# Kernel optimization log

Hardware: AMD Instinct MI355X
Metric: run time of the kernel (lower is better)

Reference implementation:

```python
import jax, jax.numpy as jnp
import numpy as np

D_MODEL = 2048
N_HEADS = 16
HEAD_DIM = D_MODEL // N_HEADS  # 128
B, S, PAST = 2, 2048, 2048


def setup_inputs() -> dict:
    key = jax.random.key(0)
    ks = jax.random.split(key, 7)
    sc = 0.02
    return {
        "x": jax.random.normal(ks[0], (B, S, D_MODEL), dtype=jnp.float32),
        "past_k": jax.random.normal(ks[1], (B, N_HEADS, PAST, HEAD_DIM), dtype=jnp.float32),
        "past_v": jax.random.normal(ks[2], (B, N_HEADS, PAST, HEAD_DIM), dtype=jnp.float32),
        "Wq": jax.random.normal(ks[3], (D_MODEL, D_MODEL), dtype=jnp.float32) * sc,
        "Wk": jax.random.normal(ks[4], (D_MODEL, D_MODEL), dtype=jnp.float32) * sc,
        "Wv": jax.random.normal(ks[5], (D_MODEL, D_MODEL), dtype=jnp.float32) * sc,
        "Wo": jax.random.normal(ks[6], (D_MODEL, D_MODEL), dtype=jnp.float32) * sc,
    }


def reference(x, past_k, past_v, Wq, Wk, Wv, Wo):
    b, s, d = x.shape
    # nn.Linear(bias=False): y = x @ W.T ; split heads -> (B, H, S, hd)
    def proj_heads(W):
        return (x @ W.T).reshape(b, s, N_HEADS, HEAD_DIM).transpose(0, 2, 1, 3)
    q = proj_heads(Wq)
    k = proj_heads(Wk)
    v = proj_heads(Wv)
    # KV-cache append along sequence axis
    k = jnp.concatenate([past_k, k], axis=2)  # (B, H, full_S, hd)
    v = jnp.concatenate([past_v, v], axis=2)
    present = (k, v)
    full_s = k.shape[2]
    scores = jnp.einsum("bhqd,bhkd->bhqk", q, k) / (HEAD_DIM ** 0.5)
    # causal mask: query i (global pos past+i) may attend keys j <= past+i
    offset = full_s - s
    qi = jnp.arange(s)[:, None]
    kj = jnp.arange(full_s)[None, :]
    mask = kj > (qi + offset)  # triu with diagonal = full_s - s + 1
    scores = jnp.where(mask[None, None], -jnp.inf, scores)
    attn = jax.nn.softmax(scores, axis=-1)
    out = jnp.einsum("bhqk,bhkd->bhqd", attn, v)
    out = out.transpose(0, 2, 1, 3).reshape(b, s, d)
    output = out @ Wo.T
    return output, present
```

## Files before the change

kernel.cpp:

```cpp
#include <hip/hip_runtime.h>
#include <hip/hip_bf16.h>
#include <stdint.h>

typedef __attribute__((ext_vector_type(8))) short bf16x8;
typedef __attribute__((ext_vector_type(4))) float f32x4;
typedef __attribute__((ext_vector_type(16))) float f32x16;
typedef unsigned short u16;
typedef unsigned int u32;
typedef const __attribute__((address_space(1))) u32* gp_t;
typedef __attribute__((address_space(3))) u32* lp_t;

#define HD 128
#define NH 16
#define SEQ 2048
#define PASTN 2048
#define FULLS 4096
#define DM 2048

__device__ __forceinline__ u16 f2b(float f){
  union { float f; u32 u; } v; v.f = f;
  return (u16)((v.u + 0x7fffu + ((v.u >> 16) & 1u)) >> 16);
}
__device__ __forceinline__ float b2f(u16 b){
  union { u32 u; float f; } v; v.u = ((u32)b) << 16;
  return v.f;
}
__device__ __forceinline__ u32 cvtpk(float lo, float hi){
  u32 r; asm("v_cvt_pk_bf16_f32 %0, %1, %2" : "=v"(r) : "v"(lo), "v"(hi)); return r;
}
__device__ __forceinline__ f32x16 zero16(){ f32x16 z = {}; return z; }

__global__ void k_conv5(const float* __restrict__ sx,
                        const float* __restrict__ s1, const float* __restrict__ s2,
                        const float* __restrict__ s3, const float* __restrict__ s4,
                        u16* __restrict__ dx,
                        u16* __restrict__ d1, u16* __restrict__ d2,
                        u16* __restrict__ d3, u16* __restrict__ d4)
{
  const int total = 2097152 + 4 * 1048576;
  int i = blockIdx.x * blockDim.x + threadIdx.x;
  int stride = gridDim.x * blockDim.x;
  for (; i < total; i += stride){
    const float* s; u16* d; int off;
    if (i < 2097152){ s = sx; d = dx; off = i; }
    else {
      int t = i - 2097152;
      int seg = t >> 20; off = t & 1048575;
      s = (seg == 0) ? s1 : (seg == 1) ? s2 : (seg == 2) ? s3 : s4;
      d = (seg == 0) ? d1 : (seg == 1) ? d2 : (seg == 2) ? d3 : d4;
    }
    float4 v = ((const float4*)s)[off];
    ushort4 o = { f2b(v.x), f2b(v.y), f2b(v.z), f2b(v.w) };
    ((ushort4*)d)[off] = o;
  }
}

__global__ __launch_bounds__(512, 1)
void k_qkv_fused(const u16* __restrict__ A,
                 const u16* __restrict__ Bq, const u16* __restrict__ Bk,
                 const u16* __restrict__ Bv,
                 u16* __restrict__ qb, u16* __restrict__ kbb,
                 u16* __restrict__ vtb,
                 float* __restrict__ outk, float* __restrict__ outv,
                 const float* __restrict__ pk, const float* __restrict__ pv)
{
  __shared__ char LDS[131072];
  const int bx = blockIdx.x;
  const int tid = threadIdx.x;

  if (bx >= 384){
    if (bx < 448){
      for (int i = (bx - 384) * 512 + tid; i < 2097152; i += 32768){
        int g = i * 4;
        int c = g & 127;
        int r = g >> 7;
        int bh = r >> 11;
        int s = r & 2047;
        long dst = ((long)bh * FULLS + s) * HD + c;
        float4 v = ((const float4*)pk)[i];
        *(float4*)(outk + dst) = v;
        ushort4 o = { f2b(v.x), f2b(v.y), f2b(v.z), f2b(v.w) };
        *(ushort4*)(kbb + dst) = o;
      }
    } else {
      float* ldsF = (float*)LDS;
      for (int cc = 0; cc < 16; cc++){
        int c = ((bx - 448) << 4) + cc;
        int bh = c >> 5, s0 = (c & 31) << 6;
        const float* src = pv + ((long)bh * PASTN + s0) * HD;
        float* dsv = outv + ((long)bh * FULLS + s0) * HD;
#pragma unroll
        for (int p = 0; p < 4; p++){
          int idx = tid + p * 512;
          int row = idx >> 5, c4 = (idx & 31) << 2;
          float4 v = *(const float4*)(src + row * HD + c4);
          *(float4*)(dsv + row * HD + c4) = v;
          ldsF[row * 129 + c4 + 0] = v.x;
          ldsF[row * 129 + c4 + 1] = v.y;
          ldsF[row * 129 + c4 + 2] = v.z;
          ldsF[row * 129 + c4 + 3] = v.w;
        }
        __syncthreads();
        int d = tid >> 2, sb = (tid & 3) << 4;
        u16* dst = vtb + ((long)bh * HD + d) * FULLS + s0 + sb;
#pragma unroll
        for (int g = 0; g < 4; g++){
          ushort4 o = { f2b(ldsF[(sb + g * 4 + 0) * 129 + d]),
                        f2b(ldsF[(sb + g * 4 + 1) * 129 + d]),
                        f2b(ldsF[(sb + g * 4 + 2) * 129 + d]),
                        f2b(ldsF[(sb + g * 4 + 3) * 129 + d]) };
          *(ushort4*)(dst + g * 4) = o;
        }
        __syncthreads();
      }
    }
    return;
  }

  const int w = tid >> 6, l = tid & 63;
  const int wm = w >> 2, wn = w & 3;
  const int which = bx >> 7;
  const int r0 = bx & 127;
  const int m0 = (r0 & 15) * 256;
  const int n0s = (r0 >> 4) * 256;
  const u16* Bm = (which == 0) ? Bq : (which == 1) ? Bk : Bv;

  const int aoff0 = (((l >> 4) * 16) ^ ((l & 7) << 4));
  const int aoff1 = ((64 + (l >> 4) * 16) ^ ((l & 7) << 4));
  const char* ArdB = LDS + wm * 16384 + (l & 15) * 128;
  const char* BrdB = LDS + 65536 + (wn >> 1) * 16384 + (wn & 1) * 8192 + (l & 15) * 128;

  const int Pa = tid * 16, Pb = tid * 16 + 8192;
  const int ra = Pa >> 7, rb = Pb >> 7;
  const int sro1 = ra * 2048 + ((((Pa & 127) ^ ((ra & 7) << 4))) >> 1);
  const int sro2 = rb * 2048 + ((((Pb & 127) ^ ((rb & 7) << 4))) >> 1);
  char* sd1 = LDS + w * 1024;
  char* sd2 = LDS + w * 1024 + 8192;

  f32x4 acc[8][4] = {};

#define GLDS(SRC, DST) __builtin_amdgcn_global_load_lds((gp_t)(const void*)(SRC), (lp_t)(void*)(DST), 16, 0, 0)
#define STG(MAT, ROWB, C, REG) { const u16* s_ = (MAT) + (long)(ROWB) * 2048 + (C) * 64; \
    GLDS(s_ + sro1, sd1 + (REG)); GLDS(s_ + sro2, sd2 + (REG)); }
#define RDB(DST, PAR) { _Pragma("unroll") for (int nf = 0; nf < 4; nf++){ \
      DST[nf*2]   = *(const bf16x8*)(BrdB + (PAR)*32768 + nf*2048 + aoff0); \
      DST[nf*2+1] = *(const bf16x8*)(BrdB + (PAR)*32768 + nf*2048 + aoff1); } }
#define RDA(PAR, MF) \
      a0 = *(const bf16x8*)(ArdB + (PAR)*32768 + (MF)*2048 + aoff0); \
      a1 = *(const bf16x8*)(ArdB + (PAR)*32768 + (MF)*2048 + aoff1); \
      a2 = *(const bf16x8*)(ArdB + (PAR)*32768 + (MF+1)*2048 + aoff0); \
      a3 = *(const bf16x8*)(ArdB + (PAR)*32768 + (MF+1)*2048 + aoff1);
#define BARW { __builtin_amdgcn_s_barrier(); \
      asm volatile("s_waitcnt lgkmcnt(0)" ::: "memory"); \
      __builtin_amdgcn_sched_barrier(0); }
#define MM(BF, MF) { __builtin_amdgcn_s_setprio(1); \
      _Pragma("unroll") for (int nf = 0; nf < 4; nf++){ \
        acc[MF][nf]   = __builtin_amdgcn_mfma_f32_16x16x32_bf16(a0, BF[nf*2],   acc[MF][nf],   0,0,0); \
        acc[MF][nf]   = __builtin_amdgcn_mfma_f32_16x16x32_bf16(a1, BF[nf*2+1], acc[MF][nf],   0,0,0); \
        acc[MF+1][nf] = __builtin_amdgcn_mfma_f32_16x16x32_bf16(a2, BF[nf*2],   acc[MF+1][nf], 0,0,0); \
        acc[MF+1][nf] = __builtin_amdgcn_mfma_f32_16x16x32_bf16(a3, BF[nf*2+1], acc[MF+1][nf], 0,0,0); } \
      __builtin_amdgcn_s_setprio(0); }

  STG(A,  m0,        0, 0);
  STG(A,  m0 + 128,  0, 16384);
  STG(Bm, n0s,       0, 65536);
  STG(Bm, n0s + 128, 0, 81920);
  STG(Bm, n0s,       1, 98304);
  STG(Bm, n0s + 128, 1, 114688);
  asm volatile("s_waitcnt vmcnt(4)" ::: "memory");
  __builtin_amdgcn_s_barrier();

  for (int i = 0; i < 16; ++i){
    const int c1 = 2 * i + 1;
    const int cn = 2 * i + 2;
    const bool nlast = (i < 15);
    bf16x8 b0[8], b1[8];
    bf16x8 a0, a1, a2, a3;

    RDB(b0, 0); RDA(0, 0);
    STG(A, m0, c1, 32768);
    BARW; MM(b0, 0);
    __builtin_amdgcn_s_barrier();

    RDA(0, 2);
    STG(A, m0 + 128, c1, 49152);
    BARW; MM(b0, 2);
    __builtin_amdgcn_s_barrier();

    RDA(0, 4);
    if (nlast) STG(Bm, n0s, cn, 65536);
    BARW; MM(b0, 4);
    __builtin_amdgcn_s_barrier();

    RDA(0, 6);
    if (nlast) STG(Bm, n0s + 128, cn, 81920);
    BARW; MM(b0, 6);
    if (nlast) { asm volatile("s_waitcnt vmcnt(4)" ::: "memory"); }
    else       { asm volatile("s_waitcnt vmcnt(0)" ::: "memory"); }
    __builtin_amdgcn_s_barrier();

    RDB(b1, 1); RDA(1, 0);
    if (nlast) STG(A, m0, cn, 0);
    BARW; MM(b1, 0);
    __builtin_amdgcn_s_barrier();

    RDA(1, 2);
    if (nlast) STG(A, m0 + 128, cn, 16384);
    BARW; MM(b1, 2);
    __builtin_amdgcn_s_barrier();

    RDA(1, 4);
    if (nlast) STG(Bm, n0s, cn + 1, 98304);
    BARW; MM(b1, 4);
    __builtin_amdgcn_s_barrier();

    RDA(1, 6);
    if (nlast) STG(Bm, n0s + 128, cn + 1, 114688);
    BARW; MM(b1, 6);
    if (nlast) { asm volatile("s_waitcnt vmcnt(4)" ::: "memory"); }
    __builtin_amdgcn_s_barrier();
  }

#undef MM
#undef BARW
#undef RDA
#undef RDB
#undef STG
#undef GLDS

  const int rbase = m0 + wm * 128 + ((l >> 4) << 2);
  const int cb2 = n0s + wn * 64 + (l & 15);
#pragma unroll
  for (int mf = 0; mf < 8; mf++){
#pragma unroll
    for (int nf = 0; nf < 4; nf++){
      const int nl = cb2 + nf * 16;
      const int h = nl >> 7, dd = nl & 127;
      if (which == 2){
        const int mm = rbase + mf * 16;
        const int b = mm >> 11, s = mm & 2047;
        const int bh = b * NH + h;
        ushort4 pkv = { f2b(acc[mf][nf][0]), f2b(acc[mf][nf][1]), f2b(acc[mf][nf][2]), f2b(acc[mf][nf][3]) };
        *(ushort4*)(vtb + ((long)bh * HD + dd) * FULLS + PASTN + s) = pkv;
#pragma unroll
        for (int r = 0; r < 4; r++){
          long idx = ((long)bh * FULLS + PASTN + s + r) * HD + dd;
          outv[idx] = acc[mf][nf][r];
        }
      } else if (which == 1){
#pragma unroll
        for (int r = 0; r < 4; r++){
          const int mm = rbase + mf * 16 + r;
          const int b = mm >> 11, s = mm & 2047;
          long idx = (((long)(b * NH + h)) * FULLS + PASTN + s) * HD + dd;
          float v = acc[mf][nf][r];
          kbb[idx] = f2b(v);
          outk[idx] = v;
        }
      } else {
#pragma unroll
        for (int r = 0; r < 4; r++){
          const int mm = rbase + mf * 16 + r;
          const int b = mm >> 11, s = mm & 2047;
          qb[(((long)(b * NH + h)) * SEQ + s) * HD + dd] = f2b(acc[mf][nf][r]);
        }
      }
    }
  }
}

__global__ __launch_bounds__(512, 1)
void k_gemm_o8(const u16* __restrict__ A, const u16* __restrict__ Bm,
               float* __restrict__ outf)
{
  __shared__ char LDS[98304];
  const int tid = threadIdx.x, w = tid >> 6, l = tid & 63;
  const int wm = w >> 2, wn = w & 3;
  const int m0 = (blockIdx.x & 15) * 256;
  const int n0 = (blockIdx.x >> 4) * 128;

  const int aoff0 = (((l >> 4) * 16) ^ ((l & 7) << 4));
  const int aoff1 = ((64 + (l >> 4) * 16) ^ ((l & 7) << 4));
  const char* ArdB = LDS + wm * 16384 + (l & 15) * 128;
  const char* BrdB = LDS + 65536 + wn * 4096 + (l & 15) * 128;

  const int Pa = tid * 16, Pb = tid * 16 + 8192;
  const int ra = Pa >> 7, rb = Pb >> 7;
  const int sro1 = ra * 2048 + ((((Pa & 127) ^ ((ra & 7) << 4))) >> 1);
  const int sro2 = rb * 2048 + ((((Pb & 127) ^ ((rb & 7) << 4))) >> 1);
  char* sd1 = LDS + w * 1024;
  char* sd2 = LDS + w * 1024 + 8192;

  f32x4 acc[8][2] = {};

#define GLDS(SRC, DST) __builtin_amdgcn_global_load_lds((gp_t)(const void*)(SRC), (lp_t)(void*)(DST), 16, 0, 0)
#define STG(MAT, ROWB, C, REG) { const u16* s_ = (MAT) + (long)(ROWB) * 2048 + (C) * 64; \
    GLDS(s_ + sro1, sd1 + (REG)); GLDS(s_ + sro2, sd2 + (REG)); }
#define RDB2(DST, PAR) { _Pragma("unroll") for (int nf = 0; nf < 2; nf++){ \
      DST[nf*2]   = *(const bf16x8*)(BrdB + (PAR)*16384 + nf*2048 + aoff0); \
      DST[nf*2+1] = *(const bf16x8*)(BrdB + (PAR)*16384 + nf*2048 + aoff1); } }
#define RDA(PAR, MF) \
      a0 = *(const bf16x8*)(ArdB + (PAR)*32768 + (MF)*2048 + aoff0); \
      a1 = *(const bf16x8*)(ArdB + (PAR)*32768 + (MF)*2048 + aoff1); \
      a2 = *(const bf16x8*)(ArdB + (PAR)*32768 + (MF+1)*2048 + aoff0); \
      a3 = *(const bf16x8*)(ArdB + (PAR)*32768 + (MF+1)*2048 + aoff1);
#define BARW { __builtin_amdgcn_s_barrier(); \
      asm volatile("s_waitcnt lgkmcnt(0)" ::: "memory"); \
      __builtin_amdgcn_sched_barrier(0); }
#define MM2(BF, MF) { __builtin_amdgcn_s_setprio(1); \
      _Pragma("unroll") for (int nf = 0; nf < 2; nf++){ \
        acc[MF][nf]   = __builtin_amdgcn_mfma_f32_16x16x32_bf16(a0, BF[nf*2],   acc[MF][nf],   0,0,0); \
        acc[MF][nf]   = __builtin_amdgcn_mfma_f32_16x16x32_bf16(a1, BF[nf*2+1], acc[MF][nf],   0,0,0); \
        acc[MF+1][nf] = __builtin_amdgcn_mfma_f32_16x16x32_bf16(a2, BF[nf*2],   acc[MF+1][nf], 0,0,0); \
        acc[MF+1][nf] = __builtin_amdgcn_mfma_f32_16x16x32_bf16(a3, BF[nf*2+1], acc[MF+1][nf], 0,0,0); } \
      __builtin_amdgcn_s_setprio(0); }

  STG(A,  m0,       0, 0);
  STG(A,  m0 + 128, 0, 16384);
  STG(Bm, n0,       0, 65536);
  STG(Bm, n0,       1, 81920);
  asm volatile("s_waitcnt vmcnt(2)" ::: "memory");
  __builtin_amdgcn_s_barrier();

  for (int i = 0; i < 16; ++i){
    const int c1 = 2 * i + 1;
    const int cn = 2 * i + 2;
    const bool nlast = (i < 15);
    bf16x8 b0[4], b1[4];
    bf16x8 a0, a1, a2, a3;

    RDB2(b0, 0); RDA(0, 0);
    STG(A, m0, c1, 32768);
    BARW; MM2(b0, 0);
    __builtin_amdgcn_s_barrier();

    RDA(0, 2);
    STG(A, m0 + 128, c1, 49152);
    BARW; MM2(b0, 2);
    __builtin_amdgcn_s_barrier();

    RDA(0, 4);
    if (nlast) STG(Bm, n0, cn, 65536);
    BARW; MM2(b0, 4);
    __builtin_amdgcn_s_barrier();

    RDA(0, 6);
    BARW; MM2(b0, 6);
    if (nlast) { asm volatile("s_waitcnt vmcnt(2)" ::: "memory"); }
    else       { asm volatile("s_waitcnt vmcnt(0)" ::: "memory"); }
    __builtin_amdgcn_s_barrier();

    RDB2(b1, 1); RDA(1, 0);
    if (nlast) STG(A, m0, cn, 0);
    BARW; MM2(b1, 0);
    __builtin_amdgcn_s_barrier();

    RDA(1, 2);
    if (nlast) STG(A, m0 + 128, cn, 16384);
    BARW; MM2(b1, 2);
    __builtin_amdgcn_s_barrier();

    RDA(1, 4);
    if (nlast) STG(Bm, n0, cn + 1, 81920);
    BARW; MM2(b1, 4);
    __builtin_amdgcn_s_barrier();

    RDA(1, 6);
    BARW; MM2(b1, 6);
    if (nlast) { asm volatile("s_waitcnt vmcnt(2)" ::: "memory"); }
    __builtin_amdgcn_s_barrier();
  }

#undef MM2
#undef BARW
#undef RDA
#undef RDB2
#undef STG
#undef GLDS

  const int rbase = m0 + wm * 128 + ((l >> 4) << 2);
  const int cb2 = n0 + wn * 32 + (l & 15);
#pragma unroll
  for (int mf = 0; mf < 8; mf++)
#pragma unroll
    for (int nf = 0; nf < 2; nf++){
      const int nn = cb2 + nf * 16;
#pragma unroll
      for (int r = 0; r < 4; r++)
        outf[(long)(rbase + mf * 16 + r) * DM + nn] = acc[mf][nf][r];
    }
}

__global__ __launch_bounds__(256, 2)
void k_attn(const u16* __restrict__ qb, const u16* __restrict__ kb,
            const u16* __restrict__ vtb, u16* __restrict__ ab)
{
  __shared__ u16 Ks[2][64 * 128];
  __shared__ u16 Vs[2][128 * 64];
  const int tid = threadIdx.x, w = tid >> 6, l = tid & 63;
  const int lq = l & 31, hi = l >> 5;
  const int dd0 = blockIdx.x;
  const int xcd = dd0 & 7;
  const int j   = dd0 >> 3;
  const int ja = j >> 5, jb = (j >> 1) & 15, jc = j & 1;
  const int bh  = xcd * 4 + 2 * ja + jc;
  const int q0b = ((ja ^ jc) ? (15 - jb) : jb) << 7;
  const int qbase = q0b + w * 32;
  const int qpos = PASTN + qbase + lq;
  const u16* qhead = qb + (long)bh * SEQ * HD;
  const u16* khead = kb + (long)bh * FULLS * HD;
  const u16* vhead = vtb + (long)bh * HD * FULLS;

  const float qscale = 0.08838834764831845f * 1.4426950408889634f;
  bf16x8 qf[8];
#pragma unroll
  for (int ks = 0; ks < 8; ks++){
    bf16x8 tq = *(const bf16x8*)(qhead + (long)(qbase + lq) * HD + ks * 16 + hi * 8);
#pragma unroll
    for (int jj = 0; jj < 8; jj++) tq[jj] = (short)f2b(b2f((u16)tq[jj]) * qscale);
    qf[ks] = tq;
  }

  const int kswz = (lq & 15) << 4;
  const int vswz = (lq & 7) << 4;
  const char* kaddr[8];
#pragma unroll
  for (int ks = 0; ks < 8; ks++)
    kaddr[ks] = (const char*)Ks + lq * 256 + ((ks * 32 + hi * 16) ^ kswz);
  const char* vaddr[4];
#pragma unroll
  for (int ks2 = 0; ks2 < 4; ks2++)
    vaddr[ks2] = (const char*)Vs + lq * 128 + ((ks2 * 32 + hi * 16) ^ vswz);

  int ksrcoff[4], vsrcoff[4];
#pragma unroll
  for (int it = 0; it < 4; it++){
    int P = it * 4096 + w * 1024 + l * 16;
    ksrcoff[it] = P ^ (((P >> 8) & 15) << 4);
    int row = P >> 7;
    int cb = (P & 127) ^ ((row & 7) << 4);
    vsrcoff[it] = row * 8192 + cb;
  }

  auto stageK = [&](int t, int bufo){
    const char* src = (const char*)khead + ((long)t << 14);
    char* dstb = (char*)Ks + bufo + w * 1024;
#pragma unroll
    for (int it = 0; it < 4; it++)
      __builtin_amdgcn_global_load_lds((gp_t)(const void*)(src + ksrcoff[it]),
                                       (lp_t)(void*)(dstb + it * 4096), 16, 0, 0);
  };
  auto stageV = [&](int t, int bufo){
    const char* src = (const char*)vhead + ((long)t << 7);
    char* dstb = (char*)Vs + bufo + w * 1024;
#pragma unroll
    for (int it = 0; it < 4; it++)
      __builtin_amdgcn_global_load_lds((gp_t)(const void*)(src + vsrcoff[it]),
                                       (lp_t)(void*)(dstb + it * 4096), 16, 0, 0);
  };

  f32x16 acc[4] = {};
  float m_run = -1e30f, l_run = 0.f;
  const int ntiles = (PASTN + q0b + 128) >> 6;

  auto finishPV = [&](f32x16& sp0, f32x16& sp1, int vbufo){
    float a0[8];
#pragma unroll
    for (int i = 0; i < 8; i++)
      a0[i] = fmaxf(fmaxf(sp0[i], sp0[i + 8]), fmaxf(sp1[i], sp1[i + 8]));
    float mx = fmaxf(fmaxf(fmaxf(a0[0], a0[1]), fmaxf(a0[2], a0[3])),
                     fmaxf(fmaxf(a0[4], a0[5]), fmaxf(a0[6], a0[7])));
    { float xa = mx, xb = mx;
      asm("v_permlane32_swap_b32 %0, %1" : "+v"(xa), "+v"(xb));
      mx = fmaxf(xa, xb); }

    if (!__all(mx <= m_run + 8.f)){
      float mnew = fmaxf(m_run, mx);
      float corr = __builtin_exp2f(m_run - mnew);
      m_run = mnew; l_run *= corr;
#pragma unroll
      for (int r = 0; r < 16; r++){
        int qlr = (r & 3) + 8 * (r >> 2) + 4 * hi;
        float cr = __shfl(corr, qlr);
#pragma unroll
        for (int d2 = 0; d2 < 4; d2++) acc[d2][r] *= cr;
      }
    }

    float rs = 0.f;
#pragma unroll
    for (int r = 0; r < 16; r++){
      sp0[r] = __builtin_exp2f(sp0[r] - m_run); rs += sp0[r];
      sp1[r] = __builtin_exp2f(sp1[r] - m_run); rs += sp1[r];
    }
    { float ra = rs, rb = rs;
      asm("v_permlane32_swap_b32 %0, %1" : "+v"(ra), "+v"(rb));
      l_run += ra + rb; }

    bf16x8 pfrag[4];
#pragma unroll
    for (int kb2 = 0; kb2 < 2; kb2++){
      const f32x16& sp = kb2 ? sp1 : sp0;
#pragma unroll
      for (int half = 0; half < 2; half++){
        const int h8 = half * 8;
        u32 A0 = cvtpk(sp[h8 + 0], sp[h8 + 1]);
        u32 A1 = cvtpk(sp[h8 + 2], sp[h8 + 3]);
        u32 B0 = cvtpk(sp[h8 + 4], sp[h8 + 5]);
        u32 B1 = cvtpk(sp[h8 + 6], sp[h8 + 7]);
        asm("v_permlane32_swap_b32 %0, %1" : "+v"(A0), "+v"(B0));
        asm("v_permlane32_swap_b32 %0, %1" : "+v"(A1), "+v"(B1));
        union { u32 wd[4]; bf16x8 v; } F;
        F.wd[0] = A0; F.wd[1] = A1; F.wd[2] = B0; F.wd[3] = B1;
        pfrag[kb2 * 2 + half] = F.v;
      }
    }

    __builtin_amdgcn_s_setprio(1);
#pragma unroll
    for (int ks2 = 0; ks2 < 4; ks2++)
#pragma unroll
      for (int d2 = 0; d2 < 4; d2++){
        bf16x8 vf = *(const bf16x8*)(vaddr[ks2] + vbufo + d2 * 4096);
        acc[d2] = __builtin_amdgcn_mfma_f32_32x32x16_bf16(pfrag[ks2], vf, acc[d2], 0, 0, 0);
      }
    __builtin_amdgcn_s_setprio(0);
  };

#define QKT_MASK(T_, BUFC_, SC0_, SC1_)                                        \
  {                                                                            \
    SC0_ = zero16(); SC1_ = zero16();                                          \
    __builtin_amdgcn_s_setprio(1);                                             \
    _Pragma("unroll")                                                          \
    for (int ks = 0; ks < 8; ks++){                                            \
      bf16x8 kf0 = *(const bf16x8*)(kaddr[ks] + (BUFC_));                      \
      bf16x8 kf1 = *(const bf16x8*)(kaddr[ks] + (BUFC_) + 8192);               \
      SC0_ = __builtin_amdgcn_mfma_f32_32x32x16_bf16(kf0, qf[ks], SC0_, 0,0,0);\
      SC1_ = __builtin_amdgcn_mfma_f32_32x32x16_bf16(kf1, qf[ks], SC1_, 0,0,0);\
    }                                                                          \
    __builtin_amdgcn_s_setprio(0);                                             \
    const int kvb_ = (T_) * 64;                                                \
    if (kvb_ + 63 > PASTN + qbase){                                            \
      _Pragma("unroll")                                                        \
      for (int r = 0; r < 16; r++){                                            \
        int key = kvb_ + (r & 3) + 8 * (r >> 2) + 4 * hi;                      \
        if (key > qpos) SC0_[r] = -1e30f;                                      \
        if (key + 32 > qpos) SC1_[r] = -1e30f;                                 \
      }                                                                        \
    }                                                                          \
  }

#define STEP(T_, BUFC_, SP0_, SP1_, SC0_, SC1_)                                \
  {                                                                            \
    if ((T_) + 1 < ntiles) stageK((T_) + 1, (BUFC_) ^ 16384);                  \
    QKT_MASK(T_, BUFC_, SC0_, SC1_);                                           \
    finishPV(SP0_, SP1_, (BUFC_) ^ 16384);                                     \
    __syncthreads();                                                           \
    if ((T_) + 1 < ntiles) stageV((T_) + 1, (BUFC_) ^ 16384);                  \
  }

  f32x16 PA0, PA1, PB0, PB1;

  stageK(0, 0); stageV(0, 0);
  __syncthreads();

  stageK(1, 16384);
  QKT_MASK(0, 0, PA0, PA1);
  __syncthreads();
  stageV(1, 16384);

  for (int t = 1; t + 2 < ntiles; t += 2){
    STEP(t,     16384, PA0, PA1, PB0, PB1);
    STEP(t + 1, 0,     PB0, PB1, PA0, PA1);
  }
  STEP(ntiles - 1, 16384, PA0, PA1, PB0, PB1);
  finishPV(PB0, PB1, 16384);

#undef STEP
#undef QKT_MASK

  float inv = 1.0f / l_run;
  const int b = bh >> 4, h = bh & 15;
#pragma unroll
  for (int r = 0; r < 16; r++){
    int qlr = (r & 3) + 8 * (r >> 2) + 4 * hi;
    float ir = __shfl(inv, qlr);
    long rowbase = ((long)b * SEQ + (qbase + qlr)) * DM + h * HD;
#pragma unroll
    for (int d2 = 0; d2 < 4; d2++)
      ab[rowbase + d2 * 32 + lq] = f2b(acc[d2][r] * ir);
  }
}

extern "C" void kernel_launch(void* const* d_in, const int* in_sizes, int n_in,
                              void* d_out, int out_size, void* d_ws, size_t ws_size,
                              hipStream_t stream) {
  const float* x      = (const float*)d_in[0];
  const float* past_k = (const float*)d_in[1];
  const float* past_v = (const float*)d_in[2];
  const float* Wq     = (const float*)d_in[3];
  const float* Wk     = (const float*)d_in[4];
  const float* Wv     = (const float*)d_in[5];
  const float* Wo     = (const float*)d_in[6];

  float* out  = (float*)d_out;
  float* outk = out + 8388608;
  float* outv = out + 25165824;

  char* ws = (char*)d_ws;
  u16* wqb = (u16*)ws;
  u16* wkb = (u16*)(ws + 8388608);
  u16* wvb = (u16*)(ws + 16777216);
  u16* wob = (u16*)(ws + 25165824);
  u16* xb  = (u16*)(ws + 33554432);
  u16* qb  = (u16*)(ws + 50331648);
  u16* kb  = (u16*)(ws + 67108864);
  u16* vtb = (u16*)(ws + 100663296);
  u16* ab  = xb;

  k_conv5<<<2048, 256, 0, stream>>>(x, Wq, Wk, Wv, Wo, xb, wqb, wkb, wvb, wob);

  k_qkv_fused<<<512, 512, 0, stream>>>(xb, wqb, wkb, wvb,
                                       qb, kb, vtb, outk, outv,
                                       past_k, past_v);

  k_attn<<<512, 256, 0, stream>>>(qb, kb, vtb, ab);

  k_gemm_o8<<<256, 512, 0, stream>>>(ab, wob, out);
}
```

Baseline: 355.7 us.

## Split attention KV range across warps with per-warp LDS buffers and merge

Restructures the attention kernel so each block handles 32 queries and its four warps each process an interleaved subset of 32-key tiles with private LDS staging, combining partial softmax states and accumulators through LDS at the end. The grid grows from 512 to 2048 blocks and block-wide barriers inside the main loop are removed. This is meant to cut inter-warp synchronisation and improve load balance and occupancy. In exchange it adds a cross-warp reduction, gives up the Q/K tile sharing across warps, and each warp loads K/V tiles with smaller MFMA batches.

```diff
diff --git a/kernel.cpp b/kernel.cpp
--- a/kernel.cpp
+++ b/kernel.cpp
@@ -395,18 +395,14 @@
 void k_attn(const u16* __restrict__ qb, const u16* __restrict__ kb,
             const u16* __restrict__ vtb, u16* __restrict__ ab)
 {
-  __shared__ u16 Ks[2][64 * 128];
-  __shared__ u16 Vs[2][128 * 64];
+  __shared__ char LDS[67584];
   const int tid = threadIdx.x, w = tid >> 6, l = tid & 63;
   const int lq = l & 31, hi = l >> 5;
-  const int dd0 = blockIdx.x;
-  const int xcd = dd0 & 7;
-  const int j   = dd0 >> 3;
-  const int ja = j >> 5, jb = (j >> 1) & 15, jc = j & 1;
-  const int bh  = xcd * 4 + 2 * ja + jc;
-  const int q0b = ((ja ^ jc) ? (15 - jb) : jb) << 7;
-  const int qbase = q0b + w * 32;
-  const int qpos = PASTN + qbase + lq;
+  const int bx = blockIdx.x;
+  const int lid = ((bx & 7) << 8) + (bx >> 3);
+  const int bh = lid >> 6;
+  const int q0 = (lid & 63) << 5;
+  const int qpos = PASTN + q0 + lq;
   const u16* qhead = qb + (long)bh * SEQ * HD;
   const u16* khead = kb + (long)bh * FULLS * HD;
   const u16* vhead = vtb + (long)bh * HD * FULLS;
@@ -415,59 +411,92 @@
   bf16x8 qf[8];
 #pragma unroll
   for (int ks = 0; ks < 8; ks++){
-    bf16x8 tq = *(const bf16x8*)(qhead + (long)(qbase + lq) * HD + ks * 16 + hi * 8);
+    bf16x8 tq = *(const bf16x8*)(qhead + (long)(q0 + lq) * HD + ks * 16 + hi * 8);
 #pragma unroll
     for (int jj = 0; jj < 8; jj++) tq[jj] = (short)f2b(b2f((u16)tq[jj]) * qscale);
     qf[ks] = tq;
   }
 
-  const int kswz = (lq & 15) << 4;
-  const int vswz = (lq & 7) << 4;
+  char* Kb = LDS + w * 16384;
+  char* Vb = Kb + 8192;
+
   const char* kaddr[8];
 #pragma unroll
   for (int ks = 0; ks < 8; ks++)
-    kaddr[ks] = (const char*)Ks + lq * 256 + ((ks * 32 + hi * 16) ^ kswz);
-  const char* vaddr[4];
-#pragma unroll
-  for (int ks2 = 0; ks2 < 4; ks2++)
-    vaddr[ks2] = (const char*)Vs + lq * 128 + ((ks2 * 32 + hi * 16) ^ vswz);
-
-  int ksrcoff[4], vsrcoff[4];
-#pragma unroll
-  for (int it = 0; it < 4; it++){
-    int P = it * 4096 + w * 1024 + l * 16;
-    ksrcoff[it] = P ^ (((P >> 8) & 15) << 4);
+    kaddr[ks] = Kb + lq * 256 + ((ks * 32 + hi * 16) ^ ((lq & 15) << 4));
+  const char* vaddr[8];
+#pragma unroll
+  for (int d2 = 0; d2 < 4; d2++){
+    int d = d2 * 32 + lq;
+    int row = d & 63;
+#pragma unroll
+    for (int ks2 = 0; ks2 < 2; ks2++){
+      int c = ((d >> 6) << 6) + ks2 * 32 + hi * 16;
+      vaddr[d2 * 2 + ks2] = Vb + row * 128 + (c ^ ((row & 7) << 4));
+    }
+  }
+
+  int ksrc[8], vsrc[8];
+#pragma unroll
+  for (int it = 0; it < 8; it++){
+    int P = it * 1024 + l * 16;
+    ksrc[it] = P ^ (((P >> 8) & 15) << 4);
     int row = P >> 7;
-    int cb = (P & 127) ^ ((row & 7) << 4);
-    vsrcoff[it] = row * 8192 + cb;
-  }
-
-  auto stageK = [&](int t, int bufo){
-    const char* src = (const char*)khead + ((long)t << 14);
-    char* dstb = (char*)Ks + bufo + w * 1024;
-#pragma unroll
-    for (int it = 0; it < 4; it++)
-      __builtin_amdgcn_global_load_lds((gp_t)(const void*)(src + ksrcoff[it]),
-                                       (lp_t)(void*)(dstb + it * 4096), 16, 0, 0);
+    int c = (P & 127) ^ ((row & 7) << 4);
+    int d = row + ((c >> 6) << 6);
+    vsrc[it] = d * FULLS + ((c & 63) >> 1);
+  }
+
+  const int ntiles = (PASTN + q0 + 32) >> 5;
+
+#define GLDS(SRC, DST) __builtin_amdgcn_global_load_lds((gp_t)(const void*)(SRC), (lp_t)(void*)(DST), 16, 0, 0)
+  auto stageK = [&](int t){
+    const char* src = (const char*)khead + ((long)t << 13);
+#pragma unroll
+    for (int it = 0; it < 8; it++)
+      GLDS(src + ksrc[it], Kb + it * 1024);
   };
-  auto stageV = [&](int t, int bufo){
-    const char* src = (const char*)vhead + ((long)t << 7);
-    char* dstb = (char*)Vs + bufo + w * 1024;
-#pragma unroll
-    for (int it = 0; it < 4; it++)
-      __builtin_amdgcn_global_load_lds((gp_t)(const void*)(src + vsrcoff[it]),
-                                       (lp_t)(void*)(dstb + it * 4096), 16, 0, 0);
+  auto stageV = [&](int t){
+    const u16* src = vhead + t * 32;
+#pragma unroll
+    for (int it = 0; it < 8; it++)
+      GLDS(src + vsrc[it], Vb + it * 1024);
   };
+#undef GLDS
 
   f32x16 acc[4] = {};
   float m_run = -1e30f, l_run = 0.f;
-  const int ntiles = (PASTN + q0b + 128) >> 6;
-
-  auto finishPV = [&](f32x16& sp0, f32x16& sp1, int vbufo){
+
+  stageK(w); stageV(w);
+
+  for (int t = w; t < ntiles; t += 4){
+    const bool more = (t + 4 < ntiles);
+
+    asm volatile("s_waitcnt vmcnt(8)" ::: "memory");
+    f32x16 s = zero16();
+    __builtin_amdgcn_s_setprio(1);
+#pragma unroll
+    for (int ks = 0; ks < 8; ks++){
+      bf16x8 kf = *(const bf16x8*)(kaddr[ks]);
+      s = __builtin_amdgcn_mfma_f32_32x32x16_bf16(kf, qf[ks], s, 0, 0, 0);
+    }
+    __builtin_amdgcn_s_setprio(0);
+    asm volatile("s_waitcnt lgkmcnt(0)" ::: "memory");
+    __builtin_amdgcn_sched_barrier(0);
+    if (more) stageK(t + 4);
+
+    const int kvb = t * 32;
+    if (kvb + 31 > PASTN + q0){
+#pragma unroll
+      for (int r = 0; r < 16; r++){
+        int key = kvb + (r & 3) + 8 * (r >> 2) + 4 * hi;
+        if (key > qpos) s[r] = -1e30f;
+      }
+    }
+
     float a0[8];
 #pragma unroll
-    for (int i = 0; i < 8; i++)
-      a0[i] = fmaxf(fmaxf(sp0[i], sp0[i + 8]), fmaxf(sp1[i], sp1[i + 8]));
+    for (int i = 0; i < 8; i++) a0[i] = fmaxf(s[i], s[i + 8]);
     float mx = fmaxf(fmaxf(fmaxf(a0[0], a0[1]), fmaxf(a0[2], a0[3])),
                      fmaxf(fmaxf(a0[4], a0[5]), fmaxf(a0[6], a0[7])));
     { float xa = mx, xb = mx;
@@ -490,105 +519,89 @@
     float rs = 0.f;
 #pragma unroll
     for (int r = 0; r < 16; r++){
-      sp0[r] = __builtin_exp2f(sp0[r] - m_run); rs += sp0[r];
-      sp1[r] = __builtin_exp2f(sp1[r] - m_run); rs += sp1[r];
+      s[r] = __builtin_exp2f(s[r] - m_run); rs += s[r];
     }
     { float ra = rs, rb = rs;
       asm("v_permlane32_swap_b32 %0, %1" : "+v"(ra), "+v"(rb));
       l_run += ra + rb; }
 
-    bf16x8 pfrag[4];
-#pragma unroll
-    for (int kb2 = 0; kb2 < 2; kb2++){
-      const f32x16& sp = kb2 ? sp1 : sp0;
-#pragma unroll
-      for (int half = 0; half < 2; half++){
-        const int h8 = half * 8;
-        u32 A0 = cvtpk(sp[h8 + 0], sp[h8 + 1]);
-        u32 A1 = cvtpk(sp[h8 + 2], sp[h8 + 3]);
-        u32 B0 = cvtpk(sp[h8 + 4], sp[h8 + 5]);
-        u32 B1 = cvtpk(sp[h8 + 6], sp[h8 + 7]);
-        asm("v_permlane32_swap_b32 %0, %1" : "+v"(A0), "+v"(B0));
-        asm("v_permlane32_swap_b32 %0, %1" : "+v"(A1), "+v"(B1));
-        union { u32 wd[4]; bf16x8 v; } F;
-        F.wd[0] = A0; F.wd[1] = A1; F.wd[2] = B0; F.wd[3] = B1;
-        pfrag[kb2 * 2 + half] = F.v;
-      }
-    }
-
+    bf16x8 pfrag[2];
+#pragma unroll
+    for (int half = 0; half < 2; half++){
+      const int h8 = half * 8;
+      u32 A0 = cvtpk(s[h8 + 0], s[h8 + 1]);
+      u32 A1 = cvtpk(s[h8 + 2], s[h8 + 3]);
+      u32 B0 = cvtpk(s[h8 + 4], s[h8 + 5]);
+      u32 B1 = cvtpk(s[h8 + 6], s[h8 + 7]);
+      asm("v_permlane32_swap_b32 %0, %1" : "+v"(A0), "+v"(B0));
+      asm("v_permlane32_swap_b32 %0, %1" : "+v"(A1), "+v"(B1));
+      union { u32 wd[4]; bf16x8 v; } F;
+      F.wd[0] = A0; F.wd[1] = A1; F.wd[2] = B0; F.wd[3] = B1;
+      pfrag[half] = F.v;
+    }
+
+    if (more) { asm volatile("s_waitcnt vmcnt(8)" ::: "memory"); }
+    else      { asm volatile("s_waitcnt vmcnt(0)" ::: "memory"); }
     __builtin_amdgcn_s_setprio(1);
 #pragma unroll
-    for (int ks2 = 0; ks2 < 4; ks2++)
+    for (int ks2 = 0; ks2 < 2; ks2++)
 #pragma unroll
       for (int d2 = 0; d2 < 4; d2++){
-        bf16x8 vf = *(const bf16x8*)(vaddr[ks2] + vbufo + d2 * 4096);
+        bf16x8 vf = *(const bf16x8*)(vaddr[d2 * 2 + ks2]);
         acc[d2] = __builtin_amdgcn_mfma_f32_32x32x16_bf16(pfrag[ks2], vf, acc[d2], 0, 0, 0);
       }
     __builtin_amdgcn_s_setprio(0);
-  };
-
-#define QKT_MASK(T_, BUFC_, SC0_, SC1_)                                        \
-  {                                                                            \
-    SC0_ = zero16(); SC1_ = zero16();                                          \
-    __builtin_amdgcn_s_setprio(1);                                             \
-    _Pragma("unroll")                                                          \
-    for (int ks = 0; ks < 8; ks++){                                            \
-      bf16x8 kf0 = *(const bf16x8*)(kaddr[ks] + (BUFC_));                      \
-      bf16x8 kf1 = *(const bf16x8*)(kaddr[ks] + (BUFC_) + 8192);               \
-      SC0_ = __builtin_amdgcn_mfma_f32_32x32x16_bf16(kf0, qf[ks], SC0_, 0,0,0);\
-      SC1_ = __builtin_amdgcn_mfma_f32_32x32x16_bf16(kf1, qf[ks], SC1_, 0,0,0);\
-    }                                                                          \
-    __builtin_amdgcn_s_setprio(0);                                             \
-    const int kvb_ = (T_) * 64;                                                \
-    if (kvb_ + 63 > PASTN + qbase){                                            \
-      _Pragma("unroll")                                                        \
-      for (int r = 0; r < 16; r++){                                            \
-        int key = kvb_ + (r & 3) + 8 * (r >> 2) + 4 * hi;                      \
-        if (key > qpos) SC0_[r] = -1e30f;                                      \
-        if (key + 32 > qpos) SC1_[r] = -1e30f;                                 \
-      }                                                                        \
-    }                                                                          \
-  }
-
-#define STEP(T_, BUFC_, SP0_, SP1_, SC0_, SC1_)                                \
-  {                                                                            \
-    if ((T_) + 1 < ntiles) stageK((T_) + 1, (BUFC_) ^ 16384);                  \
-    QKT_MASK(T_, BUFC_, SC0_, SC1_);                                           \
-    finishPV(SP0_, SP1_, (BUFC_) ^ 16384);                                     \
-    __syncthreads();                                                           \
-    if ((T_) + 1 < ntiles) stageV((T_) + 1, (BUFC_) ^ 16384);                  \
-  }
-
-  f32x16 PA0, PA1, PB0, PB1;
-
-  stageK(0, 0); stageV(0, 0);
+    asm volatile("s_waitcnt lgkmcnt(0)" ::: "memory");
+    __builtin_amdgcn_sched_barrier(0);
+    if (more) stageV(t + 4);
+  }
+
   __syncthreads();
-
-  stageK(1, 16384);
-  QKT_MASK(0, 0, PA0, PA1);
+  float* stats = (float*)(LDS + 65536);
+  stats[w * 128 + l * 2]     = m_run;
+  stats[w * 128 + l * 2 + 1] = l_run;
   __syncthreads();
-  stageV(1, 16384);
-
-  for (int t = 1; t + 2 < ntiles; t += 2){
-    STEP(t,     16384, PA0, PA1, PB0, PB1);
-    STEP(t + 1, 0,     PB0, PB1, PA0, PA1);
-  }
-  STEP(ntiles - 1, 16384, PA0, PA1, PB0, PB1);
-  finishPV(PB0, PB1, 16384);
-
-#undef STEP
-#undef QKT_MASK
-
-  float inv = 1.0f / l_run;
+
+  float mstar = -1e30f;
+#pragma unroll
+  for (int v = 0; v < 4; v++) mstar = fmaxf(mstar, stats[v * 128 + l * 2]);
+  float lstar = 0.f;
+#pragma unroll
+  for (int v = 0; v < 4; v++)
+    lstar += stats[v * 128 + l * 2 + 1] * __builtin_exp2f(stats[v * 128 + l * 2] - mstar);
+  const float sc  = __builtin_exp2f(m_run - mstar);
+  const float inv = 1.0f / lstar;
+
+#pragma unroll
+  for (int rg = 0; rg < 4; rg++){
+    float s0 = __shfl(sc, rg * 8 + 0 + 4 * hi);
+    float s1 = __shfl(sc, rg * 8 + 1 + 4 * hi);
+    float s2 = __shfl(sc, rg * 8 + 2 + 4 * hi);
+    float s3 = __shfl(sc, rg * 8 + 3 + 4 * hi);
+#pragma unroll
+    for (int d2 = 0; d2 < 4; d2++){
+      f32x4 vv = { acc[d2][rg * 4 + 0] * s0, acc[d2][rg * 4 + 1] * s1,
+                   acc[d2][rg * 4 + 2] * s2, acc[d2][rg * 4 + 3] * s3 };
+      *(f32x4*)(LDS + w * 16384 + d2 * 4096 + rg * 1024 + l * 16) = vv;
+    }
+  }
+  __syncthreads();
+
   const int b = bh >> 4, h = bh & 15;
 #pragma unroll
-  for (int r = 0; r < 16; r++){
-    int qlr = (r & 3) + 8 * (r >> 2) + 4 * hi;
-    float ir = __shfl(inv, qlr);
-    long rowbase = ((long)b * SEQ + (qbase + qlr)) * DM + h * HD;
-#pragma unroll
-    for (int d2 = 0; d2 < 4; d2++)
-      ab[rowbase + d2 * 32 + lq] = f2b(acc[d2][r] * ir);
+  for (int rg = 0; rg < 4; rg++){
+    f32x4 sum = {};
+#pragma unroll
+    for (int v = 0; v < 4; v++){
+      f32x4 p = *(const f32x4*)(LDS + v * 16384 + w * 4096 + rg * 1024 + l * 16);
+      sum[0] += p[0]; sum[1] += p[1]; sum[2] += p[2]; sum[3] += p[3];
+    }
+#pragma unroll
+    for (int j = 0; j < 4; j++){
+      int qlr = j + 8 * rg + 4 * hi;
+      float invr = __shfl(inv, qlr);
+      ab[((long)b * SEQ + q0 + qlr) * DM + h * HD + w * 32 + lq] = f2b(sum[j] * invr);
+    }
   }
 }
 
@@ -624,7 +637,7 @@
                                        qb, kb, vtb, outk, outv,
                                        past_k, past_v);
 
-  k_attn<<<512, 256, 0, stream>>>(qb, kb, vtb, ab);
+  k_attn<<<2048, 256, 0, stream>>>(qb, kb, vtb, ab);
 
   k_gemm_o8<<<256, 512, 0, stream>>>(ab, wob, out);
 }
```

After: 406.1 us. 14.2% more time.
